# Performance work log

Hardware: AMD Instinct MI355X
Metric: run time of the kernel (lower is better)

The kernel has to match this reference:

```python
import jax, jax.numpy as jnp
from jax import lax
import numpy as np

B, L, H, V = 256, 2048, 128, 32000
THR = 0.4      # energy_threshold
LN_EPS = 1e-5  # torch LayerNorm default


def setup_inputs() -> dict:
    key = jax.random.key(0)
    ks = jax.random.split(key, 12)
    s = lambda k, shp, scale: (jax.random.normal(k, shp, dtype=jnp.float32) * scale)
    return {
        "seq": jax.random.randint(ks[0], (B, L), 0, V),
        "embed": s(ks[1], (V, H), 0.02),
        "W1": s(ks[2], (H, 2 * H), H ** -0.5),
        "b1": jnp.zeros((2 * H,), jnp.float32),
        "W2": s(ks[3], (2 * H, H), (2 * H) ** -0.5),
        "b2": jnp.zeros((H,), jnp.float32),
        "gamma": jnp.ones((H,), jnp.float32),
        "beta": jnp.zeros((H,), jnp.float32),
        "Wrp": s(ks[4], (H, H), H ** -0.5),
        "brp": jnp.zeros((H,), jnp.float32),
        "Wout": s(ks[5], (H, V), H ** -0.5),
        "bout": jnp.zeros((V,), jnp.float32),
    }


def _encode(seq, embed, W1, b1, W2, b2, gamma, beta):
    e = embed[seq]                                         # [B,L,H]
    ff = jnp.maximum(e @ W1 + b1, 0.0) @ W2 + b2           # [B,L,H]
    y = e + ff
    mu = y.mean(-1, keepdims=True)
    var = ((y - mu) ** 2).mean(-1, keepdims=True)
    return (y - mu) * lax.rsqrt(var + LN_EPS) * gamma + beta


def reference(seq, embed, W1, b1, W2, b2, gamma, beta, Wrp, brp, Wout, bout):
    h_all = _encode(seq, embed, W1, b1, W2, b2, gamma, beta)  # [B,L,H]

    def step(M, k):
        # k = v = h_all[:, t, :]  -> [B,H]
        v = k
        vp = jnp.einsum('bij,bj->bi', M, k)
        error = v - vp / (jnp.sum(k * k, axis=-1, keepdims=True) + 1e-6)
        gate = (jnp.linalg.norm(error, axis=-1)
                > THR * jnp.linalg.norm(v, axis=-1)).astype(M.dtype)  # [B]
        M = M + gate[:, None, None] * jnp.einsum('bi,bj->bij', error, k)
        return M, None

    M0 = jnp.zeros((B, H, H), h_all.dtype)
    ks = jnp.swapaxes(h_all[:, :-1, :], 0, 1)               # [L-1,B,H]
    M_fin, _ = lax.scan(step, M0, ks)
    r = jnp.einsum('bij,bj->bi', M_fin, h_all[:, -1, :])    # [B,H]
    return (r @ Wrp + brp) @ Wout + bout                    # [B,V]
```

## Files before the change

kernel.cpp:

```cpp
#include <hip/hip_runtime.h>
#include <hip/hip_bf16.h>


#define BB 256
#define LL 2048
#define HH 128
#define VV 32000
#define RS 136

typedef float f32x2 __attribute__((ext_vector_type(2)));

__device__ __forceinline__ void dma16(const float* g, float* l) {
  __builtin_amdgcn_global_load_lds(
      (const __attribute__((address_space(1))) void*)g,
      (__attribute__((address_space(3))) void*)l,
      16, 0, 0);
}

template <int CTRL>
__device__ __forceinline__ float dppadd(float x) {
  int y = __builtin_amdgcn_update_dpp(0, __float_as_int(x), CTRL, 0xF, 0xF, true);
  return x + __int_as_float(y);
}

__device__ __forceinline__ void pkfma(f32x2& d, f32x2 a, f32x2 b) {
  asm("v_pk_fma_f32 %0, %1, %2, %0" : "+v"(d) : "v"(a), "v"(b));
}

__device__ __forceinline__ void barrier_lgkm() {
  asm volatile("s_waitcnt lgkmcnt(0)\n\ts_barrier" ::: "memory");
}
__device__ __forceinline__ void wait_vm1() {
  asm volatile("s_waitcnt vmcnt(1)" ::: "memory");
}
__device__ __forceinline__ void wait_vm0() {
  asm volatile("s_waitcnt vmcnt(0)" ::: "memory");
}

__global__ __launch_bounds__(256, 1) void build_htab_kernel(
    const float* __restrict__ embed,
    const float* __restrict__ W1,
    const float* __restrict__ b1,
    const float* __restrict__ W2,
    const float* __restrict__ b2,
    const float* __restrict__ gamma,
    const float* __restrict__ beta,
    float* __restrict__ Htab2)
{
  const int tid = threadIdx.x;
  const int j   = tid & 127;
  const int h2  = tid >> 7;

  float w1r[128];
#pragma unroll
  for (int m = 0; m < 128; ++m) w1r[m] = W1[m * 256 + tid];

  const float b1n = b1[tid];
  const float b2j = b2[j];
  const float gj  = gamma[j];
  const float bj  = beta[j];

  __shared__ __align__(16) float4 w2q[64][128];
  __shared__ __align__(16) float e_s[128];
  __shared__ __align__(16) float a_s[256];
  __shared__ float p_s[2][128];
  __shared__ float red[8];

  for (int idx = tid; idx < 8192; idx += 256) {
    int n4 = idx >> 7, jj = idx & 127;
    float4 w;
    w.x = W2[(size_t)(4 * n4 + 0) * 128 + jj];
    w.y = W2[(size_t)(4 * n4 + 1) * 128 + jj];
    w.z = W2[(size_t)(4 * n4 + 2) * 128 + jj];
    w.w = W2[(size_t)(4 * n4 + 3) * 128 + jj];
    w2q[n4][jj] = w;
  }
  __syncthreads();

  for (int v = blockIdx.x; v < VV; v += gridDim.x) {
    if (tid < 128) e_s[tid] = embed[(size_t)v * 128 + tid];
    __syncthreads();

    float acc[4] = {b1n, 0.f, 0.f, 0.f};
#pragma unroll
    for (int q = 0; q < 32; ++q) {
      float4 ev = *(const float4*)&e_s[4 * q];
      float t = ev.x * w1r[4 * q + 0];
      t = fmaf(ev.y, w1r[4 * q + 1], t);
      t = fmaf(ev.z, w1r[4 * q + 2], t);
      t = fmaf(ev.w, w1r[4 * q + 3], t);
      acc[q & 3] += t;
    }
    float a = fmaxf((acc[0] + acc[1]) + (acc[2] + acc[3]), 0.0f);
    a_s[tid] = a;
    __syncthreads();

    float p0 = 0.f, p1 = 0.f, p2v = 0.f, p3 = 0.f;
#pragma unroll
    for (int q = 0; q < 32; ++q) {
      int n4 = h2 * 32 + q;
      float4 av = *(const float4*)&a_s[4 * n4];
      float4 wq = w2q[n4][j];
      p0 = fmaf(av.x, wq.x, p0);
      p1 = fmaf(av.y, wq.y, p1);
      p2v = fmaf(av.z, wq.z, p2v);
      p3 = fmaf(av.w, wq.w, p3);
    }
    p_s[h2][j] = (p0 + p1) + (p2v + p3);
    __syncthreads();

    float y = 0.0f;
    if (tid < 128) {
      float ff = p_s[0][tid] + p_s[1][tid] + b2j;
      y = e_s[tid] + ff;
    }
    float s1 = y, s2 = y * y;
    s1 = dppadd<0xB1>(s1);  s2 = dppadd<0xB1>(s2);
    s1 = dppadd<0x4E>(s1);  s2 = dppadd<0x4E>(s2);
    s1 = dppadd<0x141>(s1); s2 = dppadd<0x141>(s2);
    s1 = dppadd<0x140>(s1); s2 = dppadd<0x140>(s2);
    s1 = dppadd<0x142>(s1); s2 = dppadd<0x142>(s2);
    s1 = dppadd<0x143>(s1); s2 = dppadd<0x143>(s2);
    if (tid < 128 && (tid & 63) == 63) {
      red[tid >> 6] = s1;
      red[2 + (tid >> 6)] = s2;
    }
    __syncthreads();
    float mu = (red[0] + red[1]) * (1.0f / 128.0f);
    float ms = (red[2] + red[3]) * (1.0f / 128.0f);
    float var = ms - mu * mu;
    float hv = 0.0f;
    if (tid < 128) {
      float dy = y - mu;
      hv = dy * (1.0f / sqrtf(var + 1e-5f)) * gj + bj;
      int ofs = tid + ((tid >> 6) << 2);
      Htab2[(size_t)v * RS + ofs] = hv;
    }
    float q2 = hv * hv;
    q2 = dppadd<0xB1>(q2);
    q2 = dppadd<0x4E>(q2);
    q2 = dppadd<0x141>(q2);
    q2 = dppadd<0x140>(q2);
    q2 = dppadd<0x142>(q2);
    q2 = dppadd<0x143>(q2);
    if (tid < 128 && (tid & 63) == 63) red[4 + (tid >> 6)] = q2;
    __syncthreads();
    if (tid == 0) {
      float kk = red[4] + red[5];
      Htab2[(size_t)v * RS + 132] = kk;
      Htab2[(size_t)v * RS + 133] = 1.0f / (kk + 1e-6f);
    }
    __syncthreads();
  }
}

__global__ __launch_bounds__(256, 1) void scan_kernel(
    const int* __restrict__ seq,
    const float* __restrict__ Htab2,
    const float* __restrict__ Wrp,
    const float* __restrict__ brp,
    float* __restrict__ rr)
{
  const int b     = blockIdx.x;
  const int tid   = threadIdx.x;
  const int i     = tid >> 1;
  const int half  = tid & 1;
  const int lane  = tid & 63;
  const int wv    = tid >> 6;
  const int iofs  = i + ((i >> 6) << 2);
  const int kbase = half * 68;

  __shared__ int seq_s[LL];
  __shared__ __align__(16) float slots[3][RS];
  __shared__ __align__(16) float red_s[3][4];
  __shared__ __align__(16) float r_s[128];
  __shared__ float p2_s[2][128];

  {
    int t0 = seq[(size_t)b * LL + 0];
    int t1 = seq[(size_t)b * LL + 1];
    if (lane < 34) {
      dma16(Htab2 + (size_t)t0 * RS + lane * 4, &slots[0][0]);
      dma16(Htab2 + (size_t)t1 * RS + lane * 4, &slots[1][0]);
    }
  }
  for (int t = tid; t < LL; t += 256) seq_s[t] = seq[(size_t)b * LL + t];
  __syncthreads();

  f32x2 M2[32];
#pragma unroll
  for (int m = 0; m < 32; ++m) M2[m] = f32x2{0.f, 0.f};

  f32x2 kA[32], kB[32];
  float kiA, kkA, invA, kiB, kkB, invB;
  {
    const float4* kp = (const float4*)&slots[0][kbase];
#pragma unroll
    for (int m = 0; m < 16; ++m) {
      float4 tq = kp[m];
      kA[2 * m]     = f32x2{tq.x, tq.y};
      kA[2 * m + 1] = f32x2{tq.z, tq.w};
    }
    kiA = slots[0][iofs];
    float2 kv = *(const float2*)&slots[0][132];
    kkA = kv.x; invA = kv.y;
#pragma unroll
    for (int m = 0; m < 32; ++m) asm volatile("" : "+v"(kA[m]));
    asm volatile("" : "+v"(kiA), "+v"(kkA), "+v"(invA));
  }

  auto step = [&](f32x2 (&kc)[32], float ki_c, float kk_c, float inv_c,
                  f32x2 (&kn)[32], float& ki_n, float& kk_n, float& inv_n,
                  int t, int p, int sn, int sd, int mode) {
    if (mode == 1) {
      int tk = seq_s[t + 2];
      if (lane < 34)
        dma16(Htab2 + (size_t)tk * RS + lane * 4, &slots[sd][0]);
    }
    f32x2 a0{0.f,0.f}, a1{0.f,0.f}, a2{0.f,0.f}, a3{0.f,0.f};
#pragma unroll
    for (int m = 0; m < 8; ++m) {
      pkfma(a0, kc[4 * m + 0], M2[4 * m + 0]);
      pkfma(a1, kc[4 * m + 1], M2[4 * m + 1]);
      pkfma(a2, kc[4 * m + 2], M2[4 * m + 2]);
      pkfma(a3, kc[4 * m + 3], M2[4 * m + 3]);
    }
    float vp = ((a0.x + a0.y) + (a1.x + a1.y)) + ((a2.x + a2.y) + (a3.x + a3.y));
    vp = dppadd<0xB1>(vp);
    float e = fmaf(-vp, inv_c, ki_c);
    float s = e * e;
    s = dppadd<0x4E>(s);
    s = dppadd<0x141>(s);
    s = dppadd<0x140>(s);
    s = dppadd<0x142>(s);
    s = dppadd<0x143>(s);
    if (lane == 63) red_s[p][wv] = s;
    barrier_lgkm();

    float4 rv = *(const float4*)red_s[p];
    if (mode == 1) wait_vm1(); else wait_vm0();
    {
      const float4* kp = (const float4*)&slots[sn][kbase];
#pragma unroll
      for (int m = 0; m < 16; ++m) {
        float4 tq = kp[m];
        kn[2 * m]     = f32x2{tq.x, tq.y};
        kn[2 * m + 1] = f32x2{tq.z, tq.w};
      }
      ki_n = slots[sn][iofs];
      float2 kv = *(const float2*)&slots[sn][132];
      kk_n = kv.x; inv_n = kv.y;
    }
    float ne2 = (rv.x + rv.y) + (rv.z + rv.w);
    float ge = (ne2 > 0.16f * kk_c) ? e : 0.0f;
    f32x2 ev{ge, ge};
#pragma unroll
    for (int m = 0; m < 32; ++m) pkfma(M2[m], ev, kc[m]);
#pragma unroll
    for (int m = 0; m < 32; ++m) asm volatile("" : "+v"(kn[m]));
    asm volatile("" : "+v"(ki_n), "+v"(kk_n), "+v"(inv_n));
  };

  for (int t = 0; t < LL - 2; t += 6) {
    step(kA, kiA, kkA, invA, kB, kiB, kkB, invB, t + 0, 0, 1, 2, 1);
    step(kB, kiB, kkB, invB, kA, kiA, kkA, invA, t + 1, 1, 2, 0, 1);
    step(kA, kiA, kkA, invA, kB, kiB, kkB, invB, t + 2, 2, 0, 1, 1);
    step(kB, kiB, kkB, invB, kA, kiA, kkA, invA, t + 3, 0, 1, 2, 1);
    step(kA, kiA, kkA, invA, kB, kiB, kkB, invB, t + 4, 1, 2, 0, 1);
    step(kB, kiB, kkB, invB, kA, kiA, kkA, invA, t + 5, 2, 0, 1, 1);
  }
  step(kA, kiA, kkA, invA, kB, kiB, kkB, invB, LL - 2, 0, 1, 2, 2);

  {
    f32x2 a0{0.f,0.f}, a1{0.f,0.f}, a2{0.f,0.f}, a3{0.f,0.f};
#pragma unroll
    for (int m = 0; m < 8; ++m) {
      pkfma(a0, kB[4 * m + 0], M2[4 * m + 0]);
      pkfma(a1, kB[4 * m + 1], M2[4 * m + 1]);
      pkfma(a2, kB[4 * m + 2], M2[4 * m + 2]);
      pkfma(a3, kB[4 * m + 3], M2[4 * m + 3]);
    }
    float vp = ((a0.x + a0.y) + (a1.x + a1.y)) + ((a2.x + a2.y) + (a3.x + a3.y));
    vp = dppadd<0xB1>(vp);
    if (half == 0) r_s[i] = vp;
  }
  __syncthreads();

  const int j  = tid & 127;
  const int h2 = tid >> 7;
  float pac[2] = {0.f, 0.f};
#pragma unroll
  for (int m = 0; m < 64; ++m) {
    pac[m & 1] = fmaf(r_s[h2 * 64 + m],
                      Wrp[(size_t)(h2 * 64 + m) * 128 + j], pac[m & 1]);
  }
  p2_s[h2][j] = pac[0] + pac[1];
  __syncthreads();
  if (tid < 128) {
    rr[(size_t)b * 128 + tid] = p2_s[0][tid] + p2_s[1][tid] + brp[tid];
  }
}

__global__ __launch_bounds__(256, 1) void out_kernel(
    const float* __restrict__ rr,
    const float* __restrict__ Wout,
    const float* __restrict__ bout,
    float* __restrict__ out)
{
  const int tid = threadIdx.x;
  const int v = blockIdx.x * 64 + (tid & 63);
  const int bg = tid >> 6;
  const int b0 = blockIdx.y * 64;

  __shared__ float4 rs4[64][32];
  for (int idx = tid; idx < 2048; idx += 256) {
    int bb = idx >> 5, q = idx & 31;
    rs4[bb][q] = ((const float4*)rr)[(size_t)(b0 + bb) * 32 + q];
  }
  __syncthreads();

  float acc[16];
#pragma unroll
  for (int m = 0; m < 16; ++m) acc[m] = 0.0f;

  for (int h4 = 0; h4 < 32; ++h4) {
    float w0 = Wout[(size_t)(4 * h4 + 0) * VV + v];
    float w1 = Wout[(size_t)(4 * h4 + 1) * VV + v];
    float w2 = Wout[(size_t)(4 * h4 + 2) * VV + v];
    float w3 = Wout[(size_t)(4 * h4 + 3) * VV + v];
#pragma unroll
    for (int m = 0; m < 16; ++m) {
      float4 rv = rs4[bg * 16 + m][h4];
      float t = rv.x * w0;
      t = fmaf(rv.y, w1, t);
      t = fmaf(rv.z, w2, t);
      t = fmaf(rv.w, w3, t);
      acc[m] += t;
    }
  }
  float bo = bout[v];
#pragma unroll
  for (int m = 0; m < 16; ++m) {
    out[(size_t)(b0 + bg * 16 + m) * VV + v] = acc[m] + bo;
  }
}

extern "C" void kernel_launch(void* const* d_in, const int* in_sizes, int n_in,
                              void* d_out, int out_size, void* d_ws, size_t ws_size,
                              hipStream_t stream)
{
  const int* seq      = (const int*)d_in[0];
  const float* embed  = (const float*)d_in[1];
  const float* W1     = (const float*)d_in[2];
  const float* b1     = (const float*)d_in[3];
  const float* W2     = (const float*)d_in[4];
  const float* b2     = (const float*)d_in[5];
  const float* gamma  = (const float*)d_in[6];
  const float* beta   = (const float*)d_in[7];
  const float* Wrp    = (const float*)d_in[8];
  const float* brp    = (const float*)d_in[9];
  const float* Wout   = (const float*)d_in[10];
  const float* bout   = (const float*)d_in[11];
  float* out          = (float*)d_out;

  char* ws = (char*)d_ws;
  float* Htab2 = (float*)ws;
  float* rr    = (float*)(ws + 17408000);

  hipLaunchKernelGGL(build_htab_kernel, dim3(256), dim3(256), 0, stream,
                     embed, W1, b1, W2, b2, gamma, beta, Htab2);
  hipLaunchKernelGGL(scan_kernel, dim3(BB), dim3(256), 0, stream,
                     seq, Htab2, Wrp, brp, rr);
  hipLaunchKernelGGL(out_kernel, dim3(VV / 64, 4), dim3(256), 0, stream,
                     rr, Wout, bout, out);
}
```

Measured before the change: 1.468 ms.

## Process scan steps in pairs with algebraic correction to halve barriers

Restructures the sequential memory-update scan to handle two timesteps per barrier. The second step's prediction error and its norm are derived algebraically from the first step's error, the dot product of the two keys and a cross term, so a single block-wide reduction and barrier serves both steps. DMA prefetch now fetches two key rows into a four-slot buffer. This cuts the per-step barrier and reduction latency in half, in exchange for roughly double the register pressure for keys, extra FMAs, and small floating-point reassociation differences that could flip a gate decision near the threshold.

```diff
diff --git a/kernel.cpp b/kernel.cpp
--- a/kernel.cpp
+++ b/kernel.cpp
@@ -30,11 +30,22 @@
 __device__ __forceinline__ void barrier_lgkm() {
   asm volatile("s_waitcnt lgkmcnt(0)\n\ts_barrier" ::: "memory");
 }
-__device__ __forceinline__ void wait_vm1() {
-  asm volatile("s_waitcnt vmcnt(1)" ::: "memory");
-}
 __device__ __forceinline__ void wait_vm0() {
   asm volatile("s_waitcnt vmcnt(0)" ::: "memory");
+}
+
+struct KSet {
+  f32x2 a[32], b[32];
+  float kia, kkA, invA, kib, kkB, invB;
+};
+
+__device__ __forceinline__ void pin(KSet& K) {
+#pragma unroll
+  for (int m = 0; m < 32; ++m) asm volatile("" : "+v"(K.a[m]));
+#pragma unroll
+  for (int m = 0; m < 32; ++m) asm volatile("" : "+v"(K.b[m]));
+  asm volatile("" : "+v"(K.kia), "+v"(K.kkA), "+v"(K.invA));
+  asm volatile("" : "+v"(K.kib), "+v"(K.kkB), "+v"(K.invB));
 }
 
 __global__ __launch_bounds__(256, 1) void build_htab_kernel(
@@ -171,8 +182,8 @@
   const int kbase = half * 68;
 
   __shared__ int seq_s[LL];
-  __shared__ __align__(16) float slots[3][RS];
-  __shared__ __align__(16) float red_s[3][4];
+  __shared__ __align__(16) float slots[4][RS];
+  __shared__ __align__(16) float red2[3][4];
   __shared__ __align__(16) float r_s[128];
   __shared__ float p2_s[2][128];
 
@@ -191,96 +202,137 @@
 #pragma unroll
   for (int m = 0; m < 32; ++m) M2[m] = f32x2{0.f, 0.f};
 
-  f32x2 kA[32], kB[32];
-  float kiA, kkA, invA, kiB, kkB, invB;
+  KSet KA, KB;
+
+  auto load_set = [&](KSet& K, int sa, int sb) {
+    const float4* pa = (const float4*)&slots[sa][kbase];
+    const float4* pb = (const float4*)&slots[sb][kbase];
+#pragma unroll
+    for (int m = 0; m < 16; ++m) {
+      float4 ta = pa[m];
+      K.a[2 * m]     = f32x2{ta.x, ta.y};
+      K.a[2 * m + 1] = f32x2{ta.z, ta.w};
+      float4 tb = pb[m];
+      K.b[2 * m]     = f32x2{tb.x, tb.y};
+      K.b[2 * m + 1] = f32x2{tb.z, tb.w};
+    }
+    K.kia = slots[sa][iofs];
+    K.kib = slots[sb][iofs];
+    float2 va = *(const float2*)&slots[sa][132];
+    float2 vb = *(const float2*)&slots[sb][132];
+    K.kkA = va.x; K.invA = va.y;
+    K.kkB = vb.x; K.invB = vb.y;
+  };
+
+  load_set(KA, 0, 1);
+  pin(KA);
+
+  auto pair_step = [&](KSet& Kc, KSet& Kn, int n, int mode) {
+    int sd = ((n + 1) & 1) * 2;
+    {
+      int ta = seq_s[2 * n + 2], tb = seq_s[2 * n + 3];
+      if (lane < 34) {
+        dma16(Htab2 + (size_t)ta * RS + lane * 4, &slots[sd][0]);
+        dma16(Htab2 + (size_t)tb * RS + lane * 4, &slots[sd + 1][0]);
+      }
+    }
+    f32x2 aa{0.f,0.f}, ab{0.f,0.f}, ba{0.f,0.f}, bb{0.f,0.f}, dd{0.f,0.f}, de{0.f,0.f};
+#pragma unroll
+    for (int m = 0; m < 16; ++m) {
+      pkfma(aa, Kc.a[2 * m],     M2[2 * m]);
+      pkfma(ab, Kc.a[2 * m + 1], M2[2 * m + 1]);
+      pkfma(ba, Kc.b[2 * m],     M2[2 * m]);
+      pkfma(bb, Kc.b[2 * m + 1], M2[2 * m + 1]);
+      pkfma(dd, Kc.a[2 * m],     Kc.b[2 * m]);
+      pkfma(de, Kc.a[2 * m + 1], Kc.b[2 * m + 1]);
+    }
+    float vpa = (aa.x + aa.y) + (ab.x + ab.y);
+    float vpb = (ba.x + ba.y) + (bb.x + bb.y);
+    float d   = (dd.x + dd.y) + (de.x + de.y);
+    vpa = dppadd<0xB1>(vpa);
+    vpb = dppadd<0xB1>(vpb);
+    d   = dppadd<0xB1>(d);
+    float ea = fmaf(-vpa, Kc.invA, Kc.kia);
+    float c  = fmaf(-vpb, Kc.invB, Kc.kib);
+    float sE = ea * ea, sC = c * c, sX = c * ea;
+    sE = dppadd<0x4E>(sE);  sC = dppadd<0x4E>(sC);  sX = dppadd<0x4E>(sX);
+    sE = dppadd<0x141>(sE); sC = dppadd<0x141>(sC); sX = dppadd<0x141>(sX);
+    sE = dppadd<0x140>(sE); sC = dppadd<0x140>(sC); sX = dppadd<0x140>(sX);
+    sE = dppadd<0x142>(sE); sC = dppadd<0x142>(sC); sX = dppadd<0x142>(sX);
+    sE = dppadd<0x143>(sE); sC = dppadd<0x143>(sC); sX = dppadd<0x143>(sX);
+    if (lane == 63) {
+      red2[0][wv] = sE;
+      red2[1][wv] = sC;
+      red2[2][wv] = sX;
+    }
+    barrier_lgkm();
+
+    float4 rE = *(const float4*)red2[0];
+    float4 rC = *(const float4*)red2[1];
+    float4 rX = *(const float4*)red2[2];
+
+    wait_vm0();
+    load_set(Kn, sd, sd + 1);
+    pin(Kn);
+
+    float SE = (rE.x + rE.y) + (rE.z + rE.w);
+    float SC = (rC.x + rC.y) + (rC.z + rC.w);
+    float SX = (rX.x + rX.y) + (rX.z + rX.w);
+    float ga = (SE > 0.16f * Kc.kkA) ? 1.0f : 0.0f;
+    float hb = ga * d * Kc.invB;
+    float eb = fmaf(-hb, ea, c);
+    float SEB = fmaf(hb * hb, SE, fmaf(-2.0f * hb, SX, SC));
+    float gea = ga * ea;
+    float geb = (SEB > 0.16f * Kc.kkB) ? eb : 0.0f;
+    f32x2 va{gea, gea}, vb{geb, geb};
+#pragma unroll
+    for (int m = 0; m < 32; ++m) {
+      pkfma(M2[m], va, Kc.a[m]);
+      pkfma(M2[m], vb, Kc.b[m]);
+    }
+    (void)mode;
+  };
+
+  for (int n = 0; n < 511; ++n) {
+    pair_step(KA, KB, 2 * n, 0);
+    pair_step(KB, KA, 2 * n + 1, 0);
+  }
+  pair_step(KA, KB, 1022, 1);
+
   {
-    const float4* kp = (const float4*)&slots[0][kbase];
+    f32x2 aa{0.f,0.f}, ab{0.f,0.f};
 #pragma unroll
     for (int m = 0; m < 16; ++m) {
-      float4 tq = kp[m];
-      kA[2 * m]     = f32x2{tq.x, tq.y};
-      kA[2 * m + 1] = f32x2{tq.z, tq.w};
-    }
-    kiA = slots[0][iofs];
-    float2 kv = *(const float2*)&slots[0][132];
-    kkA = kv.x; invA = kv.y;
-#pragma unroll
-    for (int m = 0; m < 32; ++m) asm volatile("" : "+v"(kA[m]));
-    asm volatile("" : "+v"(kiA), "+v"(kkA), "+v"(invA));
-  }
-
-  auto step = [&](f32x2 (&kc)[32], float ki_c, float kk_c, float inv_c,
-                  f32x2 (&kn)[32], float& ki_n, float& kk_n, float& inv_n,
-                  int t, int p, int sn, int sd, int mode) {
-    if (mode == 1) {
-      int tk = seq_s[t + 2];
-      if (lane < 34)
-        dma16(Htab2 + (size_t)tk * RS + lane * 4, &slots[sd][0]);
-    }
-    f32x2 a0{0.f,0.f}, a1{0.f,0.f}, a2{0.f,0.f}, a3{0.f,0.f};
-#pragma unroll
-    for (int m = 0; m < 8; ++m) {
-      pkfma(a0, kc[4 * m + 0], M2[4 * m + 0]);
-      pkfma(a1, kc[4 * m + 1], M2[4 * m + 1]);
-      pkfma(a2, kc[4 * m + 2], M2[4 * m + 2]);
-      pkfma(a3, kc[4 * m + 3], M2[4 * m + 3]);
-    }
-    float vp = ((a0.x + a0.y) + (a1.x + a1.y)) + ((a2.x + a2.y) + (a3.x + a3.y));
+      pkfma(aa, KB.a[2 * m],     M2[2 * m]);
+      pkfma(ab, KB.a[2 * m + 1], M2[2 * m + 1]);
+    }
+    float vp = (aa.x + aa.y) + (ab.x + ab.y);
     vp = dppadd<0xB1>(vp);
-    float e = fmaf(-vp, inv_c, ki_c);
+    float e = fmaf(-vp, KB.invA, KB.kia);
     float s = e * e;
     s = dppadd<0x4E>(s);
     s = dppadd<0x141>(s);
     s = dppadd<0x140>(s);
     s = dppadd<0x142>(s);
     s = dppadd<0x143>(s);
-    if (lane == 63) red_s[p][wv] = s;
-    barrier_lgkm();
-
-    float4 rv = *(const float4*)red_s[p];
-    if (mode == 1) wait_vm1(); else wait_vm0();
-    {
-      const float4* kp = (const float4*)&slots[sn][kbase];
-#pragma unroll
-      for (int m = 0; m < 16; ++m) {
-        float4 tq = kp[m];
-        kn[2 * m]     = f32x2{tq.x, tq.y};
-        kn[2 * m + 1] = f32x2{tq.z, tq.w};
-      }
-      ki_n = slots[sn][iofs];
-      float2 kv = *(const float2*)&slots[sn][132];
-      kk_n = kv.x; inv_n = kv.y;
-    }
+    if (lane == 63) red2[0][wv] = s;
+    __syncthreads();
+    float4 rv = *(const float4*)red2[0];
     float ne2 = (rv.x + rv.y) + (rv.z + rv.w);
-    float ge = (ne2 > 0.16f * kk_c) ? e : 0.0f;
+    float ge = (ne2 > 0.16f * KB.kkA) ? e : 0.0f;
     f32x2 ev{ge, ge};
 #pragma unroll
-    for (int m = 0; m < 32; ++m) pkfma(M2[m], ev, kc[m]);
-#pragma unroll
-    for (int m = 0; m < 32; ++m) asm volatile("" : "+v"(kn[m]));
-    asm volatile("" : "+v"(ki_n), "+v"(kk_n), "+v"(inv_n));
-  };
-
-  for (int t = 0; t < LL - 2; t += 6) {
-    step(kA, kiA, kkA, invA, kB, kiB, kkB, invB, t + 0, 0, 1, 2, 1);
-    step(kB, kiB, kkB, invB, kA, kiA, kkA, invA, t + 1, 1, 2, 0, 1);
-    step(kA, kiA, kkA, invA, kB, kiB, kkB, invB, t + 2, 2, 0, 1, 1);
-    step(kB, kiB, kkB, invB, kA, kiA, kkA, invA, t + 3, 0, 1, 2, 1);
-    step(kA, kiA, kkA, invA, kB, kiB, kkB, invB, t + 4, 1, 2, 0, 1);
-    step(kB, kiB, kkB, invB, kA, kiA, kkA, invA, t + 5, 2, 0, 1, 1);
-  }
-  step(kA, kiA, kkA, invA, kB, kiB, kkB, invB, LL - 2, 0, 1, 2, 2);
+    for (int m = 0; m < 32; ++m) pkfma(M2[m], ev, KB.a[m]);
+  }
 
   {
-    f32x2 a0{0.f,0.f}, a1{0.f,0.f}, a2{0.f,0.f}, a3{0.f,0.f};
-#pragma unroll
-    for (int m = 0; m < 8; ++m) {
-      pkfma(a0, kB[4 * m + 0], M2[4 * m + 0]);
-      pkfma(a1, kB[4 * m + 1], M2[4 * m + 1]);
-      pkfma(a2, kB[4 * m + 2], M2[4 * m + 2]);
-      pkfma(a3, kB[4 * m + 3], M2[4 * m + 3]);
-    }
-    float vp = ((a0.x + a0.y) + (a1.x + a1.y)) + ((a2.x + a2.y) + (a3.x + a3.y));
+    f32x2 aa{0.f,0.f}, ab{0.f,0.f};
+#pragma unroll
+    for (int m = 0; m < 16; ++m) {
+      pkfma(aa, KB.b[2 * m],     M2[2 * m]);
+      pkfma(ab, KB.b[2 * m + 1], M2[2 * m + 1]);
+    }
+    float vp = (aa.x + aa.y) + (ab.x + ab.y);
     vp = dppadd<0xB1>(vp);
     if (half == 0) r_s[i] = vp;
   }
```

Result: slower. 1.598 ms (+8.9%).

## Run one scan sequence per wavefront with M rows held in registers, no block barriers

Applied to the files above, without the earlier changes.

The scan kernel moves from one 256-thread block per batch row (M split over 4 waves and joined through LDS reductions and barriers) to a single wavefront per batch row. Each lane holds two full rows of M (256 floats) in registers, and the gate reduction becomes DPP plus readlane, so the per-step block barrier goes away. The M update is skipped whenever the gate is off. The Htab row layout drops its padding and a 4-slot DMA ring prefetches two steps ahead. The costs are very high VGPR pressure (likely spills), only 128 blocks of 128 threads on the GPU, and the key being reread from LDS for both the matvec and the update.

```diff
diff --git a/kernel.cpp b/kernel.cpp
--- a/kernel.cpp
+++ b/kernel.cpp
@@ -7,6 +7,7 @@
 #define HH 128
 #define VV 32000
 #define RS 136
+#define WSS 256
 
 typedef float f32x2 __attribute__((ext_vector_type(2)));
 
@@ -27,14 +28,14 @@
   asm("v_pk_fma_f32 %0, %1, %2, %0" : "+v"(d) : "v"(a), "v"(b));
 }
 
-__device__ __forceinline__ void barrier_lgkm() {
-  asm volatile("s_waitcnt lgkmcnt(0)\n\ts_barrier" ::: "memory");
-}
-__device__ __forceinline__ void wait_vm1() {
-  asm volatile("s_waitcnt vmcnt(1)" ::: "memory");
-}
 __device__ __forceinline__ void wait_vm0() {
   asm volatile("s_waitcnt vmcnt(0)" ::: "memory");
+}
+__device__ __forceinline__ void wait_vm2() {
+  asm volatile("s_waitcnt vmcnt(2)" ::: "memory");
+}
+__device__ __forceinline__ void wait_lgkm0() {
+  asm volatile("s_waitcnt lgkmcnt(0)" ::: "memory");
 }
 
 __global__ __launch_bounds__(256, 1) void build_htab_kernel(
@@ -133,8 +134,7 @@
     if (tid < 128) {
       float dy = y - mu;
       hv = dy * (1.0f / sqrtf(var + 1e-5f)) * gj + bj;
-      int ofs = tid + ((tid >> 6) << 2);
-      Htab2[(size_t)v * RS + ofs] = hv;
+      Htab2[(size_t)v * RS + tid] = hv;
     }
     float q2 = hv * hv;
     q2 = dppadd<0xB1>(q2);
@@ -147,158 +147,137 @@
     __syncthreads();
     if (tid == 0) {
       float kk = red[4] + red[5];
-      Htab2[(size_t)v * RS + 132] = kk;
-      Htab2[(size_t)v * RS + 133] = 1.0f / (kk + 1e-6f);
-    }
-    __syncthreads();
-  }
-}
-
-__global__ __launch_bounds__(256, 1) void scan_kernel(
+      Htab2[(size_t)v * RS + 128] = kk;
+      Htab2[(size_t)v * RS + 129] = 1.0f / (kk + 1e-6f);
+    }
+    __syncthreads();
+  }
+}
+
+__global__ __launch_bounds__(128, 1) void scan_kernel(
     const int* __restrict__ seq,
     const float* __restrict__ Htab2,
     const float* __restrict__ Wrp,
     const float* __restrict__ brp,
     float* __restrict__ rr)
 {
-  const int b     = blockIdx.x;
-  const int tid   = threadIdx.x;
-  const int i     = tid >> 1;
-  const int half  = tid & 1;
-  const int lane  = tid & 63;
-  const int wv    = tid >> 6;
-  const int iofs  = i + ((i >> 6) << 2);
-  const int kbase = half * 68;
-
-  __shared__ int seq_s[LL];
-  __shared__ __align__(16) float slots[3][RS];
-  __shared__ __align__(16) float red_s[3][4];
-  __shared__ __align__(16) float r_s[128];
-  __shared__ float p2_s[2][128];
+  const int tid  = threadIdx.x;
+  const int lane = tid & 63;
+  const int wv   = tid >> 6;
+  const int b    = blockIdx.x * 2 + wv;
+
+  __shared__ int seq_s[2][LL];
+  __shared__ __align__(16) float slots[2][4][WSS];
+  __shared__ __align__(16) float rbuf[2][128];
+
+  int*   sq   = seq_s[wv];
+  float* slot = &slots[wv][0][0];
+
+  for (int i = lane; i < LL; i += 64) sq[i] = seq[(size_t)b * LL + i];
 
   {
     int t0 = seq[(size_t)b * LL + 0];
     int t1 = seq[(size_t)b * LL + 1];
-    if (lane < 34) {
-      dma16(Htab2 + (size_t)t0 * RS + lane * 4, &slots[0][0]);
-      dma16(Htab2 + (size_t)t1 * RS + lane * 4, &slots[1][0]);
-    }
-  }
-  for (int t = tid; t < LL; t += 256) seq_s[t] = seq[(size_t)b * LL + t];
-  __syncthreads();
-
-  f32x2 M2[32];
-#pragma unroll
-  for (int m = 0; m < 32; ++m) M2[m] = f32x2{0.f, 0.f};
-
-  f32x2 kA[32], kB[32];
-  float kiA, kkA, invA, kiB, kkB, invB;
-  {
-    const float4* kp = (const float4*)&slots[0][kbase];
-#pragma unroll
-    for (int m = 0; m < 16; ++m) {
-      float4 tq = kp[m];
-      kA[2 * m]     = f32x2{tq.x, tq.y};
-      kA[2 * m + 1] = f32x2{tq.z, tq.w};
-    }
-    kiA = slots[0][iofs];
-    float2 kv = *(const float2*)&slots[0][132];
-    kkA = kv.x; invA = kv.y;
-#pragma unroll
-    for (int m = 0; m < 32; ++m) asm volatile("" : "+v"(kA[m]));
-    asm volatile("" : "+v"(kiA), "+v"(kkA), "+v"(invA));
-  }
-
-  auto step = [&](f32x2 (&kc)[32], float ki_c, float kk_c, float inv_c,
-                  f32x2 (&kn)[32], float& ki_n, float& kk_n, float& inv_n,
-                  int t, int p, int sn, int sd, int mode) {
-    if (mode == 1) {
-      int tk = seq_s[t + 2];
-      if (lane < 34)
-        dma16(Htab2 + (size_t)tk * RS + lane * 4, &slots[sd][0]);
-    }
-    f32x2 a0{0.f,0.f}, a1{0.f,0.f}, a2{0.f,0.f}, a3{0.f,0.f};
-#pragma unroll
-    for (int m = 0; m < 8; ++m) {
-      pkfma(a0, kc[4 * m + 0], M2[4 * m + 0]);
-      pkfma(a1, kc[4 * m + 1], M2[4 * m + 1]);
-      pkfma(a2, kc[4 * m + 2], M2[4 * m + 2]);
-      pkfma(a3, kc[4 * m + 3], M2[4 * m + 3]);
-    }
-    float vp = ((a0.x + a0.y) + (a1.x + a1.y)) + ((a2.x + a2.y) + (a3.x + a3.y));
-    vp = dppadd<0xB1>(vp);
-    float e = fmaf(-vp, inv_c, ki_c);
-    float s = e * e;
+    dma16(Htab2 + (size_t)t0 * RS + lane * 4, slot);
+    dma16(Htab2 + (size_t)t1 * RS + lane * 4, slot + WSS);
+  }
+  wait_vm0();
+  wait_lgkm0();
+
+  f32x2 m0[64], m1[64];
+#pragma unroll
+  for (int c = 0; c < 64; ++c) {
+    m0[c] = f32x2{0.f, 0.f};
+    m1[c] = f32x2{0.f, 0.f};
+  }
+
+  for (int t = 0; t < LL - 1; ++t) {
+    int tn = t + 2; if (tn > LL - 1) tn = LL - 1;
+    int tok = sq[tn];
+    dma16(Htab2 + (size_t)tok * RS + lane * 4, slot + ((t + 2) & 3) * WSS);
+    wait_vm2();
+    asm volatile("" ::: "memory");
+
+    const float*  sl = slot + (t & 3) * WSS;
+    const float4* kp = (const float4*)sl;
+    f32x2 kown = *(const f32x2*)(sl + 2 * lane);
+    float kk  = sl[128];
+    float inv = sl[129];
+
+    f32x2 a00{0.f,0.f}, a01{0.f,0.f}, a10{0.f,0.f}, a11{0.f,0.f};
+#pragma unroll
+    for (int c = 0; c < 32; ++c) {
+      float4 kq = kp[c];
+      f32x2 kA{kq.x, kq.y}, kB{kq.z, kq.w};
+      pkfma(a00, m0[2 * c],     kA);
+      pkfma(a01, m0[2 * c + 1], kB);
+      pkfma(a10, m1[2 * c],     kA);
+      pkfma(a11, m1[2 * c + 1], kB);
+    }
+    float vp0 = (a00.x + a00.y) + (a01.x + a01.y);
+    float vp1 = (a10.x + a10.y) + (a11.x + a11.y);
+    float e0 = fmaf(-vp0, inv, kown.x);
+    float e1 = fmaf(-vp1, inv, kown.y);
+    float s = fmaf(e0, e0, e1 * e1);
+    s = dppadd<0xB1>(s);
     s = dppadd<0x4E>(s);
     s = dppadd<0x141>(s);
     s = dppadd<0x140>(s);
     s = dppadd<0x142>(s);
     s = dppadd<0x143>(s);
-    if (lane == 63) red_s[p][wv] = s;
-    barrier_lgkm();
-
-    float4 rv = *(const float4*)red_s[p];
-    if (mode == 1) wait_vm1(); else wait_vm0();
-    {
-      const float4* kp = (const float4*)&slots[sn][kbase];
-#pragma unroll
-      for (int m = 0; m < 16; ++m) {
-        float4 tq = kp[m];
-        kn[2 * m]     = f32x2{tq.x, tq.y};
-        kn[2 * m + 1] = f32x2{tq.z, tq.w};
+    float ne2 = __int_as_float(__builtin_amdgcn_readlane(__float_as_int(s), 63));
+    if (ne2 > 0.16f * kk) {
+      f32x2 ev0{e0, e0}, ev1{e1, e1};
+#pragma unroll
+      for (int c = 0; c < 32; ++c) {
+        float4 kq = kp[c];
+        f32x2 kA{kq.x, kq.y}, kB{kq.z, kq.w};
+        pkfma(m0[2 * c],     ev0, kA);
+        pkfma(m0[2 * c + 1], ev0, kB);
+        pkfma(m1[2 * c],     ev1, kA);
+        pkfma(m1[2 * c + 1], ev1, kB);
       }
-      ki_n = slots[sn][iofs];
-      float2 kv = *(const float2*)&slots[sn][132];
-      kk_n = kv.x; inv_n = kv.y;
-    }
-    float ne2 = (rv.x + rv.y) + (rv.z + rv.w);
-    float ge = (ne2 > 0.16f * kk_c) ? e : 0.0f;
-    f32x2 ev{ge, ge};
-#pragma unroll
-    for (int m = 0; m < 32; ++m) pkfma(M2[m], ev, kc[m]);
-#pragma unroll
-    for (int m = 0; m < 32; ++m) asm volatile("" : "+v"(kn[m]));
-    asm volatile("" : "+v"(ki_n), "+v"(kk_n), "+v"(inv_n));
-  };
-
-  for (int t = 0; t < LL - 2; t += 6) {
-    step(kA, kiA, kkA, invA, kB, kiB, kkB, invB, t + 0, 0, 1, 2, 1);
-    step(kB, kiB, kkB, invB, kA, kiA, kkA, invA, t + 1, 1, 2, 0, 1);
-    step(kA, kiA, kkA, invA, kB, kiB, kkB, invB, t + 2, 2, 0, 1, 1);
-    step(kB, kiB, kkB, invB, kA, kiA, kkA, invA, t + 3, 0, 1, 2, 1);
-    step(kA, kiA, kkA, invA, kB, kiB, kkB, invB, t + 4, 1, 2, 0, 1);
-    step(kB, kiB, kkB, invB, kA, kiA, kkA, invA, t + 5, 2, 0, 1, 1);
-  }
-  step(kA, kiA, kkA, invA, kB, kiB, kkB, invB, LL - 2, 0, 1, 2, 2);
-
+    }
+  }
+
+  wait_vm0();
   {
-    f32x2 a0{0.f,0.f}, a1{0.f,0.f}, a2{0.f,0.f}, a3{0.f,0.f};
-#pragma unroll
-    for (int m = 0; m < 8; ++m) {
-      pkfma(a0, kB[4 * m + 0], M2[4 * m + 0]);
-      pkfma(a1, kB[4 * m + 1], M2[4 * m + 1]);
-      pkfma(a2, kB[4 * m + 2], M2[4 * m + 2]);
-      pkfma(a3, kB[4 * m + 3], M2[4 * m + 3]);
-    }
-    float vp = ((a0.x + a0.y) + (a1.x + a1.y)) + ((a2.x + a2.y) + (a3.x + a3.y));
-    vp = dppadd<0xB1>(vp);
-    if (half == 0) r_s[i] = vp;
-  }
-  __syncthreads();
-
-  const int j  = tid & 127;
-  const int h2 = tid >> 7;
-  float pac[2] = {0.f, 0.f};
-#pragma unroll
-  for (int m = 0; m < 64; ++m) {
-    pac[m & 1] = fmaf(r_s[h2 * 64 + m],
-                      Wrp[(size_t)(h2 * 64 + m) * 128 + j], pac[m & 1]);
-  }
-  p2_s[h2][j] = pac[0] + pac[1];
-  __syncthreads();
-  if (tid < 128) {
-    rr[(size_t)b * 128 + tid] = p2_s[0][tid] + p2_s[1][tid] + brp[tid];
-  }
+    const float*  sl = slot + ((LL - 1) & 3) * WSS;
+    const float4* kp = (const float4*)sl;
+    f32x2 a00{0.f,0.f}, a01{0.f,0.f}, a10{0.f,0.f}, a11{0.f,0.f};
+#pragma unroll
+    for (int c = 0; c < 32; ++c) {
+      float4 kq = kp[c];
+      f32x2 kA{kq.x, kq.y}, kB{kq.z, kq.w};
+      pkfma(a00, m0[2 * c],     kA);
+      pkfma(a01, m0[2 * c + 1], kB);
+      pkfma(a10, m1[2 * c],     kA);
+      pkfma(a11, m1[2 * c + 1], kB);
+    }
+    float vp0 = (a00.x + a00.y) + (a01.x + a01.y);
+    float vp1 = (a10.x + a10.y) + (a11.x + a11.y);
+    ((f32x2*)rbuf[wv])[lane] = f32x2{vp0, vp1};
+  }
+  wait_lgkm0();
+
+  f32x2 acc{0.f, 0.f};
+  const float4* rbp = (const float4*)rbuf[wv];
+#pragma unroll 8
+  for (int m4 = 0; m4 < 32; ++m4) {
+    float4 rq = rbp[m4];
+    const float* wp = &Wrp[(size_t)(4 * m4) * 128 + 2 * lane];
+    f32x2 w0 = *(const f32x2*)(wp);
+    f32x2 w1 = *(const f32x2*)(wp + 128);
+    f32x2 w2 = *(const f32x2*)(wp + 256);
+    f32x2 w3 = *(const f32x2*)(wp + 384);
+    pkfma(acc, w0, f32x2{rq.x, rq.x});
+    pkfma(acc, w1, f32x2{rq.y, rq.y});
+    pkfma(acc, w2, f32x2{rq.z, rq.z});
+    pkfma(acc, w3, f32x2{rq.w, rq.w});
+  }
+  f32x2 bp = *(const f32x2*)&brp[2 * lane];
+  f32x2 res; res.x = acc.x + bp.x; res.y = acc.y + bp.y;
+  *(f32x2*)&rr[(size_t)b * 128 + 2 * lane] = res;
 }
 
 __global__ __launch_bounds__(256, 1) void out_kernel(
@@ -365,11 +344,11 @@
 
   char* ws = (char*)d_ws;
   float* Htab2 = (float*)ws;
-  float* rr    = (float*)(ws + 17408000);
+  float* rr    = (float*)(ws + 17412096);
 
   hipLaunchKernelGGL(build_htab_kernel, dim3(256), dim3(256), 0, stream,
                      embed, W1, b1, W2, b2, gamma, beta, Htab2);
-  hipLaunchKernelGGL(scan_kernel, dim3(BB), dim3(256), 0, stream,
+  hipLaunchKernelGGL(scan_kernel, dim3(BB / 2), dim3(128), 0, stream,
                      seq, Htab2, Wrp, brp, rr);
   hipLaunchKernelGGL(out_kernel, dim3(VV / 64, 4), dim3(256), 0, stream,
                      rr, Wout, bout, out);
```

Measured after the change: 3.564 ms. +142.8%, slower.
